# Kernel optimization log

Measured on AMD Instinct MI355X. Metric: run time of the kernel, lower is better.

Reference implementation:

```python
import jax, jax.numpy as jnp
import numpy as np

B, N_OBS = 4096, 64
H = 256
SCALE = 0.05  # keep activations stable through SQUARE/MUL layers


def setup_inputs() -> dict:
    key = jax.random.key(0)
    ks = jax.random.split(key, 16)
    rn = lambda k, shp, s=SCALE: s * jax.random.normal(k, shp, dtype=jnp.float32)
    return {
        "x": jax.random.normal(ks[0], (B, N_OBS), dtype=jnp.float32),
        "xdot": jax.random.normal(ks[1], (B, N_OBS), dtype=jnp.float32),
        "w1": rn(ks[2], (H, N_OBS)), "b1": rn(ks[3], (H,)),
        "w2a": rn(ks[4], (H, H)), "b2a": rn(ks[5], (H,)),
        "w2b": rn(ks[6], (H, H)), "b2b": rn(ks[7], (H,)),
        "w3a": rn(ks[8], (H, H)), "b3a": rn(ks[9], (H,)),
        "w3s": rn(ks[10], (H, N_OBS)), "b3s": rn(ks[11], (H,)),
        "wout": rn(ks[12], (1, H)),
        "scalar": jax.random.normal(ks[13], (1,), dtype=jnp.float32),
    }


def reference(x, xdot, w1, b1, w2a, b2a, w2b, b2b, w3a, b3a, w3s, b3s, wout, scalar):
    # mul path: empty mul_activation -> yy = x*0 + scalar  (shape [B, n_obs])
    yy = x * 0 + scalar

    # Layer 1: SQUARE. Initial jac is identity, so
    # matmul(2*diag(z), W1) @ I == 2*z[:,:,None] * W1
    z = x @ w1.T + b1                      # [B, H]
    y = z * z
    jac = (2.0 * z)[:, :, None] * w1[None]  # [B, H, N_OBS]

    # Layer 2: MUL. diag(z1)@W2b + diag(z2)@W2a == z1[:,:,None]*w2b + z2[:,:,None]*w2a
    z1 = y @ w2a.T + b2a
    z2 = y @ w2b.T + b2b
    y = z1 * z2
    grad = z1[:, :, None] * w2b[None] + z2[:, :, None] * w2a[None]  # [B, H, H]
    jac = jnp.einsum('boh,bhi->boi', grad, jac)                      # [B, H, N_OBS]

    # Layer 3: SKIP. jac = diag(z1)@W3s + (diag(z2)@W3a)@jac
    z1 = y @ w3a.T + b3a
    z2 = x @ w3s.T + b3s
    y = z1 * z2
    jac = z1[:, :, None] * w3s[None] + z2[:, :, None] * jnp.einsum('oh,bhi->boi', w3a, jac)

    numerical_b = y @ wout.T                                # [B, 1]
    jac = jnp.einsum('oh,bhi->boi', wout, jac)              # [B, 1, N_OBS]
    numerical_bdot = jnp.sum(jac[:, 0, :] * xdot, axis=1)   # [B]
    return (numerical_b, numerical_bdot, y, yy)
```

## Files before the change

kernel.cpp:

```cpp
#include <hip/hip_runtime.h>

typedef unsigned short ushort_t;
typedef unsigned int uint_t;
typedef __bf16 bf16x8 __attribute__((ext_vector_type(8)));
typedef float f32x4 __attribute__((ext_vector_type(4)));

#define H 256
#define RPB 16
#define NBLK 256

#define NB_OFF 0
#define BDOT_OFF 4096
#define Y_OFF 8192
#define YY_OFF (8192 + 4096 * 256)

__device__ __forceinline__ ushort_t f2bf(float x) {
    union { float f; uint_t u; } c; c.f = x;
    uint_t r = (c.u + 0x7FFFu + ((c.u >> 16) & 1u)) >> 16;
    return (ushort_t)r;
}
__device__ __forceinline__ float bf2f(ushort_t v) {
    union { uint_t u; float f; } c; c.u = ((uint_t)v) << 16;
    return c.f;
}

#define O_W1b  0
#define O_W1T  16384
#define O_W2ab 32768
#define O_W2bb 98304
#define O_W3ab 163840
#define O_W2aT 229376
#define O_W2bT 294912
#define O_W3aT 360448
#define O_W3sb 425984
#define O_W3sT 442368

__global__ __launch_bounds__(256) void prep_weights(
    const float* __restrict__ w1, const float* __restrict__ w2a,
    const float* __restrict__ w2b, const float* __restrict__ w3a,
    const float* __restrict__ w3s, const float* __restrict__ wout,
    ushort_t* __restrict__ ws) {
    __shared__ float tile[32][65];
    int b = blockIdx.x;
    const float* src; int Oo, Ot, C, t; bool scl;
    if (b < 32)       { src = w2a; Oo = O_W2ab; Ot = O_W2aT; C = 256; t = b;       scl = false; }
    else if (b < 64)  { src = w2b; Oo = O_W2bb; Ot = O_W2bT; C = 256; t = b - 32;  scl = false; }
    else if (b < 96)  { src = w3a; Oo = O_W3ab; Ot = O_W3aT; C = 256; t = b - 64;  scl = true;  }
    else if (b < 104) { src = w1;  Oo = O_W1b;  Ot = O_W1T;  C = 64;  t = b - 96;  scl = false; }
    else              { src = w3s; Oo = O_W3sb; Ot = O_W3sT; C = 64;  t = b - 104; scl = true;  }
    int tr, tc;
    if (C == 256) { tr = t >> 2; tc = t & 3; } else { tr = t; tc = 0; }
    int r0 = tr * 32, c0 = tc * 64;
    const int tid = threadIdx.x;

    union pack8 { ushort_t u[8]; uint4 q; };
    {
        int r = tid >> 3, c8 = (tid & 7) << 3;
        const float* s = src + (r0 + r) * C + c0 + c8;
        pack8 p;
#pragma unroll
        for (int j = 0; j < 8; j++) { float v = s[j]; tile[r][c8 + j] = v; p.u[j] = f2bf(v); }
        *(uint4*)(ws + Oo + (r0 + r) * C + c0 + c8) = p.q;
    }
    __syncthreads();
    {
        int cc = tid >> 2, r8 = (tid & 3) << 3;
        pack8 p;
#pragma unroll
        for (int j = 0; j < 8; j++) {
            float v = tile[r8 + j][cc];
            if (scl) v *= wout[r0 + r8 + j];
            p.u[j] = f2bf(v);
        }
        *(uint4*)(ws + Ot + (c0 + cc) * 256 + r0 + r8) = p.q;
    }
}

#define U_BA   0
#define U_BB   16384
#define U_Z    32768
#define U_Y    36864
#define U_Z12  40960
#define U_Z22  45056
#define U_Z13  49152
#define U_Z23  53248
#define U_U    57344
#define U_XD   61440
#define U_NB   63488
#define SMEM_USHORTS 63520
#define SMEM_BYTES (SMEM_USHORTS * 2)

__device__ __forceinline__ void gload16(const ushort_t* g, ushort_t* l) {
    __builtin_amdgcn_global_load_lds(
        (const __attribute__((address_space(1))) void*)g,
        (__attribute__((address_space(3))) void*)l, 16, 0, 0);
}

__device__ __forceinline__ int posw(int r, int c) { return r * H + (c ^ ((r & 7) << 3)); }

template <bool SUM>
__device__ __forceinline__ void staged_dual(
    const ushort_t* __restrict__ g0, const ushort_t* __restrict__ g1,
    const ushort_t* sA0, const ushort_t* sA1,
    ushort_t* sB0, ushort_t* sB1,
    int wid, int lane, f32x4& acc0, f32x4& acc1) {
    const int nsrc = (wid << 4) + (lane >> 2);
    const int osrc = ((lane & 3) ^ (nsrc & 3)) << 3;
    const ushort_t* s0 = g0 + nsrc * 256 + osrc;
    const ushort_t* s1 = g1 + nsrc * 256 + osrc;
    const int dstb = wid << 9;
    const int row = lane & 15;
    const int nn = (wid << 4) + row;
    const int kq = (lane >> 4) << 3;
    const int boff = nn * 32 + (kq ^ ((nn & 3) << 3));
    const int sw = (row & 7) << 3;
    const ushort_t* a0p = sA0 + row * 256;
    const ushort_t* a1p = sA1 + row * 256;

    asm volatile("s_waitcnt vmcnt(0)" ::: "memory");
    gload16(s0, sB0 + dstb);
    gload16(s1, sB1 + dstb);
    gload16(s0 + 32, sB0 + 8192 + dstb);
    gload16(s1 + 32, sB1 + 8192 + dstb);
#pragma unroll
    for (int c = 0; c < 8; ++c) {
        if (c < 7) asm volatile("s_waitcnt vmcnt(2)" ::: "memory");
        else       asm volatile("s_waitcnt vmcnt(0)" ::: "memory");
        const int cb = (c & 1) << 13;
        bf16x8 a0 = *(const bf16x8*)(a0p + (((c << 5) + kq) ^ sw));
        bf16x8 b0 = *(const bf16x8*)(sB0 + cb + boff);
        bf16x8 a1 = *(const bf16x8*)(a1p + (((c << 5) + kq) ^ sw));
        bf16x8 b1 = *(const bf16x8*)(sB1 + cb + boff);
        if (c < 6) {
            asm volatile("s_waitcnt lgkmcnt(0)" ::: "memory");
            gload16(s0 + (c + 2) * 32, sB0 + cb + dstb);
            gload16(s1 + (c + 2) * 32, sB1 + cb + dstb);
        }
        acc0 = __builtin_amdgcn_mfma_f32_16x16x32_bf16(a0, b0, acc0, 0, 0, 0);
        if (SUM)
            acc0 = __builtin_amdgcn_mfma_f32_16x16x32_bf16(a1, b1, acc0, 0, 0, 0);
        else
            acc1 = __builtin_amdgcn_mfma_f32_16x16x32_bf16(a1, b1, acc1, 0, 0, 0);
    }
}

template <int NF, int STRA, int STRB>
__device__ __forceinline__ void gemm_one(const ushort_t* sA, const ushort_t* __restrict__ B0,
                                         int lane, int k0, f32x4& acc0) {
    const int row = lane & 15;
    const int kq = (lane >> 4) << 3;
    const int sw = (row & 7) << 3;
    bf16x8 b0[NF], a[NF];
    const ushort_t* bp0 = B0 + row * STRB + k0 + kq;
    const ushort_t* ap = sA + row * STRA;
#pragma unroll
    for (int i = 0; i < NF; i++) b0[i] = *(const bf16x8*)(bp0 + i * 32);
#pragma unroll
    for (int i = 0; i < NF; i++) a[i] = *(const bf16x8*)(ap + ((k0 + i * 32 + kq) ^ sw));
    __builtin_amdgcn_sched_barrier(0);
#pragma unroll
    for (int i = 0; i < NF; i++)
        acc0 = __builtin_amdgcn_mfma_f32_16x16x32_bf16(a[i], b0[i], acc0, 0, 0, 0);
}

__global__ __launch_bounds__(1024) void net_main(
    const float* __restrict__ x, const float* __restrict__ xd,
    const float* __restrict__ b1, const float* __restrict__ b2a,
    const float* __restrict__ b2b, const float* __restrict__ b3a,
    const float* __restrict__ b3s, const float* __restrict__ wout,
    const float* __restrict__ scalar, const ushort_t* __restrict__ ws,
    float* __restrict__ out) {
    extern __shared__ __align__(16) ushort_t smem[];
    ushort_t* sBA = smem + U_BA;
    ushort_t* sBB = smem + U_BB;
    ushort_t* sZ  = smem + U_Z;
    ushort_t* sY  = smem + U_Y;
    ushort_t* sZ12 = smem + U_Z12;
    ushort_t* sZ22 = smem + U_Z22;
    ushort_t* sZ13 = smem + U_Z13;
    ushort_t* sZ23 = smem + U_Z23;
    ushort_t* sU  = smem + U_U;
    float* sXd = (float*)(smem + U_XD);
    float* sNB = (float*)(smem + U_NB);

    const int tid = threadIdx.x;
    const int wid = tid >> 6;
    const int lane = tid & 63;
    const int row16 = lane & 15;
    const int rq = lane >> 4;
    const int R0 = blockIdx.x * RPB;
    const int n0 = wid * 16;
    const int row = lane & 15;
    const int kq = (lane >> 4) << 3;
    const int sw = (row & 7) << 3;

    {
        const ushort_t* w1p = ws + O_W1b + (n0 + row) * 64 + kq;
        const ushort_t* w3p = ws + O_W3sb + (n0 + row) * 64 + kq;
        bf16x8 pb0 = *(const bf16x8*)(w1p);
        bf16x8 pb1 = *(const bf16x8*)(w1p + 32);
        bf16x8 pb2 = *(const bf16x8*)(w3p);
        bf16x8 pb3 = *(const bf16x8*)(w3p + 32);
        const float* xg = x + (R0 + row) * 64;
        float4 x0 = *(const float4*)(xg + kq);
        float4 x1 = *(const float4*)(xg + kq + 4);
        float4 x2 = *(const float4*)(xg + 32 + kq);
        float4 x3 = *(const float4*)(xg + 32 + kq + 4);
        float sc = scalar[0];
        {
            int r = tid >> 6, c = tid & 63;
            sXd[tid] = xd[(R0 + r) * 64 + c];
            out[YY_OFF + (R0 + r) * 64 + c] = sc;
            if (tid < RPB) sNB[tid] = 0.f;
        }
        union { ushort_t u[8]; bf16x8 v; } A0, A1;
#pragma unroll
        for (int j = 0; j < 4; j++) {
            A0.u[j]     = f2bf(((const float*)&x0)[j]);
            A0.u[4 + j] = f2bf(((const float*)&x1)[j]);
            A1.u[j]     = f2bf(((const float*)&x2)[j]);
            A1.u[4 + j] = f2bf(((const float*)&x3)[j]);
        }
        f32x4 z = {0.f,0.f,0.f,0.f}, q = {0.f,0.f,0.f,0.f};
        z = __builtin_amdgcn_mfma_f32_16x16x32_bf16(A0.v, pb0, z, 0, 0, 0);
        z = __builtin_amdgcn_mfma_f32_16x16x32_bf16(A1.v, pb1, z, 0, 0, 0);
        q = __builtin_amdgcn_mfma_f32_16x16x32_bf16(A0.v, pb2, q, 0, 0, 0);
        q = __builtin_amdgcn_mfma_f32_16x16x32_bf16(A1.v, pb3, q, 0, 0, 0);
        int c = n0 + row16;
        float bz = b1[c], bs = b3s[c];
#pragma unroll
        for (int i = 0; i < 4; i++) {
            int r = rq * 4 + i;
            int p = posw(r, c);
            float za = z[i] + bz;
            sZ[p] = f2bf(za);
            sY[p] = f2bf(za * za);
            sZ23[p] = f2bf(q[i] + bs);
        }
    }
    __syncthreads();

    {
        f32x4 aA = {0.f,0.f,0.f,0.f}, aB = {0.f,0.f,0.f,0.f};
        staged_dual<false>(ws + O_W2ab, ws + O_W2bb, sY, sY, sBA, sBB, wid, lane, aA, aB);
        int c = n0 + row16;
        float ba = b2a[c], bb = b2b[c];
#pragma unroll
        for (int i = 0; i < 4; i++) {
            int r = rq * 4 + i;
            int p = posw(r, c);
            float z12 = aA[i] + ba, z22 = aB[i] + bb;
            sZ12[p] = f2bf(z12);
            sZ22[p] = f2bf(z22);
            sU[p] = f2bf(z12 * z22);
        }
    }
    __syncthreads();

    {
        f32x4 zz = {0.f,0.f,0.f,0.f}, tt = {0.f,0.f,0.f,0.f};
        staged_dual<false>(ws + O_W3ab, ws + O_W3aT, sU, sZ23, sBA, sBB, wid, lane, zz, tt);
        int c = n0 + row16;
        float ba = b3a[c], wo = wout[c];
#pragma unroll
        for (int i = 0; i < 4; i++) {
            int r = rq * 4 + i;
            int p = posw(r, c);
            float z13 = zz[i] + ba;
            float z23 = bf2f(sZ23[p]);
            float y3 = z13 * z23;
            out[Y_OFF + (R0 + r) * H + c] = y3;
            sZ13[p] = f2bf(z13);
            float t = tt[i];
            sZ12[p] = f2bf(t * bf2f(sZ12[p]));
            sZ22[p] = f2bf(t * bf2f(sZ22[p]));
            float v = wo * y3;
            v += __shfl_xor(v, 1);
            v += __shfl_xor(v, 2);
            v += __shfl_xor(v, 4);
            v += __shfl_xor(v, 8);
            if (row16 == 0) atomicAdd(&sNB[r], v);
        }
    }
    __syncthreads();

    {
        f32x4 pp = {0.f,0.f,0.f,0.f}, dummy = {0.f,0.f,0.f,0.f};
        staged_dual<true>(ws + O_W2bT, ws + O_W2aT, sZ12, sZ22, sBA, sBB, wid, lane, pp, dummy);
        int c = n0 + row16;
#pragma unroll
        for (int i = 0; i < 4; i++) {
            int r = rq * 4 + i;
            int p = posw(r, c);
            sZ[p] = f2bf(2.f * pp[i] * bf2f(sZ[p]));
        }
    }
    __syncthreads();

    {
        int mat = wid >> 3, kh = (wid >> 2) & 1, nt = wid & 3;
        const ushort_t* A = mat ? sZ : sZ13;
        const ushort_t* B = ws + (mat ? O_W1T : O_W3sT) + nt * 16 * H;
        f32x4 acc = {0.f,0.f,0.f,0.f};
        gemm_one<4, H, H>(A, B, lane, kh * 128, acc);
        float* dst = mat ? ((float*)sU + kh * 1024) : ((float*)sY + kh * 1024);
        int c = nt * 16 + row16;
#pragma unroll
        for (int i = 0; i < 4; i++) dst[(rq * 4 + i) * 64 + c] = acc[i];
    }
    __syncthreads();

    {
        float* F0 = (float*)sY;
        float* F1 = F0 + 1024;
        float* F2 = (float*)sU;
        float* F3 = F2 + 1024;
        int r = tid >> 6, j = tid & 63;
        int e = r * 64 + j;
        float s = (F0[e] + F1[e] + F2[e] + F3[e]) * sXd[e];
        s += __shfl_xor(s, 1);
        s += __shfl_xor(s, 2);
        s += __shfl_xor(s, 4);
        s += __shfl_xor(s, 8);
        s += __shfl_xor(s, 16);
        s += __shfl_xor(s, 32);
        if (j == 0) out[BDOT_OFF + R0 + r] = s;
        if (tid < RPB) out[NB_OFF + R0 + tid] = sNB[tid];
    }
}

extern "C" void kernel_launch(void* const* d_in, const int* in_sizes, int n_in,
                              void* d_out, int out_size, void* d_ws, size_t ws_size,
                              hipStream_t stream) {
    (void)in_sizes; (void)n_in; (void)out_size; (void)ws_size;
    const float* x = (const float*)d_in[0];
    const float* xd = (const float*)d_in[1];
    const float* w1 = (const float*)d_in[2];
    const float* b1 = (const float*)d_in[3];
    const float* w2a = (const float*)d_in[4];
    const float* b2a = (const float*)d_in[5];
    const float* w2b = (const float*)d_in[6];
    const float* b2b = (const float*)d_in[7];
    const float* w3a = (const float*)d_in[8];
    const float* b3a = (const float*)d_in[9];
    const float* w3s = (const float*)d_in[10];
    const float* b3s = (const float*)d_in[11];
    const float* wout = (const float*)d_in[12];
    const float* scalar = (const float*)d_in[13];
    ushort_t* ws = (ushort_t*)d_ws;
    float* out = (float*)d_out;

    static bool attr_set = false;
    if (!attr_set) {
        hipFuncSetAttribute((const void*)net_main,
                            hipFuncAttributeMaxDynamicSharedMemorySize, SMEM_BYTES);
        attr_set = true;
    }

    prep_weights<<<112, 256, 0, stream>>>(w1, w2a, w2b, w3a, w3s, wout, ws);
    net_main<<<NBLK, 1024, SMEM_BYTES, stream>>>(x, xd, b1, b2a, b2b, b3a, b3s, wout, scalar, ws, out);
}
```

Baseline: 30.51 us.

## Replace per-phase double-buffered weight staging with cross-phase per-wave LDS ring

Swaps the per-phase double-buffered shared staging of weight tiles for a per-wave five-slot LDS ring that keeps four 16-byte async global-to-LDS loads in flight. The ring runs continuously across the three GEMM phases, so the next phase's weights are prefetched while the current phase computes. The first weight loads are issued before layer 1, and the y3 global store is deferred to the end of the kernel. __syncthreads is replaced by a lighter lgkmcnt wait plus a raw s_barrier. The goal is to hide global-load latency and phase-start stalls, at the cost of more LDS use and fragile hand-managed vmcnt accounting.

Result: slower. 31.21 us (+2.3%).

```diff
diff --git a/kernel.cpp b/kernel.cpp
--- a/kernel.cpp
+++ b/kernel.cpp
@@ -76,18 +76,18 @@
     }
 }
 
-#define U_BA   0
-#define U_BB   16384
-#define U_Z    32768
-#define U_Y    36864
-#define U_Z12  40960
-#define U_Z22  45056
-#define U_Z13  49152
-#define U_Z23  53248
-#define U_U    57344
-#define U_XD   61440
-#define U_NB   63488
-#define SMEM_USHORTS 63520
+#define RS 5
+#define RA 4
+#define U_RING 0
+#define U_Z    40960
+#define U_Y    45056
+#define U_Z12  49152
+#define U_Z22  53248
+#define U_Z23  57344
+#define U_U    61440
+#define U_XD   65536
+#define U_NB   69632
+#define SMEM_USHORTS 69664
 #define SMEM_BYTES (SMEM_USHORTS * 2)
 
 __device__ __forceinline__ void gload16(const ushort_t* g, ushort_t* l) {
@@ -96,51 +96,59 @@
         (__attribute__((address_space(3))) void*)l, 16, 0, 0);
 }
 
+template <int N> __device__ __forceinline__ void vwait() {
+    if constexpr (N == 3) asm volatile("s_waitcnt vmcnt(3)" ::: "memory");
+    else if constexpr (N == 2) asm volatile("s_waitcnt vmcnt(2)" ::: "memory");
+    else if constexpr (N == 1) asm volatile("s_waitcnt vmcnt(1)" ::: "memory");
+    else asm volatile("s_waitcnt vmcnt(0)" ::: "memory");
+}
+
+#define PHASE_BARRIER() do { \
+    asm volatile("s_waitcnt lgkmcnt(0)" ::: "memory"); \
+    __builtin_amdgcn_sched_barrier(0); \
+    __builtin_amdgcn_s_barrier(); \
+    __builtin_amdgcn_sched_barrier(0); \
+} while (0)
+
 __device__ __forceinline__ int posw(int r, int c) { return r * H + (c ^ ((r & 7) << 3)); }
 
-template <bool SUM>
-__device__ __forceinline__ void staged_dual(
-    const ushort_t* __restrict__ g0, const ushort_t* __restrict__ g1,
-    const ushort_t* sA0, const ushort_t* sA1,
-    ushort_t* sB0, ushort_t* sB1,
-    int wid, int lane, f32x4& acc0, f32x4& acc1) {
-    const int nsrc = (wid << 4) + (lane >> 2);
-    const int osrc = ((lane & 3) ^ (nsrc & 3)) << 3;
-    const ushort_t* s0 = g0 + nsrc * 256 + osrc;
-    const ushort_t* s1 = g1 + nsrc * 256 + osrc;
-    const int dstb = wid << 9;
-    const int row = lane & 15;
-    const int nn = (wid << 4) + row;
-    const int kq = (lane >> 4) << 3;
-    const int boff = nn * 32 + (kq ^ ((nn & 3) << 3));
-    const int sw = (row & 7) << 3;
-    const ushort_t* a0p = sA0 + row * 256;
-    const ushort_t* a1p = sA1 + row * 256;
-
-    asm volatile("s_waitcnt vmcnt(0)" ::: "memory");
-    gload16(s0, sB0 + dstb);
-    gload16(s1, sB1 + dstb);
-    gload16(s0 + 32, sB0 + 8192 + dstb);
-    gload16(s1 + 32, sB1 + 8192 + dstb);
-#pragma unroll
-    for (int c = 0; c < 8; ++c) {
-        if (c < 7) asm volatile("s_waitcnt vmcnt(2)" ::: "memory");
-        else       asm volatile("s_waitcnt vmcnt(0)" ::: "memory");
-        const int cb = (c & 1) << 13;
-        bf16x8 a0 = *(const bf16x8*)(a0p + (((c << 5) + kq) ^ sw));
-        bf16x8 b0 = *(const bf16x8*)(sB0 + cb + boff);
-        bf16x8 a1 = *(const bf16x8*)(a1p + (((c << 5) + kq) ^ sw));
-        bf16x8 b1 = *(const bf16x8*)(sB1 + cb + boff);
-        if (c < 6) {
-            asm volatile("s_waitcnt lgkmcnt(0)" ::: "memory");
-            gload16(s0 + (c + 2) * 32, sB0 + cb + dstb);
-            gload16(s1 + (c + 2) * 32, sB1 + cb + dstb);
-        }
-        acc0 = __builtin_amdgcn_mfma_f32_16x16x32_bf16(a0, b0, acc0, 0, 0, 0);
+template <int P, bool SUM>
+__device__ __forceinline__ void ring_phase(
+    const ushort_t* __restrict__ gm0, const ushort_t* __restrict__ gm1,
+    const ushort_t* __restrict__ gn0, const ushort_t* __restrict__ gn1,
+    const ushort_t* aP0, const ushort_t* aP1,
+    ushort_t* rw, int srcoff, int boff, int kq, int sw,
+    f32x4& acc0, f32x4& acc1) {
+#pragma unroll
+    for (int k = 0; k < 16; ++k) {
+        const int u = P * 16 + k;
+        if (P == 2) {
+            if (k < 13) vwait<3>();
+            else if (k == 13) vwait<2>();
+            else if (k == 14) vwait<1>();
+            else vwait<0>();
+        } else {
+            vwait<3>();
+        }
+        __builtin_amdgcn_sched_barrier(0);
+        bf16x8 b = *(const bf16x8*)(rw + (u % RS) * 512 + boff);
+        const ushort_t* ap = (k & 1) ? aP1 : aP0;
+        bf16x8 a = *(const bf16x8*)(ap + ((((k >> 1) << 5) + kq) ^ sw));
+        if (u + RA < 48) {
+            asm volatile("s_waitcnt lgkmcnt(2)" ::: "memory");
+            __builtin_amdgcn_sched_barrier(0);
+            const int k4 = k + RA;
+            const ushort_t* g = (k4 < 16) ? ((k4 & 1) ? gm1 : gm0)
+                                          : ((k4 & 1) ? gn1 : gn0);
+            const int cc = (k4 & 15) >> 1;
+            gload16(g + srcoff + (cc << 5), rw + ((u + RA) % RS) * 512);
+        }
         if (SUM)
-            acc0 = __builtin_amdgcn_mfma_f32_16x16x32_bf16(a1, b1, acc0, 0, 0, 0);
+            acc0 = __builtin_amdgcn_mfma_f32_16x16x32_bf16(a, b, acc0, 0, 0, 0);
+        else if ((k & 1) == 0)
+            acc0 = __builtin_amdgcn_mfma_f32_16x16x32_bf16(a, b, acc0, 0, 0, 0);
         else
-            acc1 = __builtin_amdgcn_mfma_f32_16x16x32_bf16(a1, b1, acc1, 0, 0, 0);
+            acc1 = __builtin_amdgcn_mfma_f32_16x16x32_bf16(a, b, acc1, 0, 0, 0);
     }
 }
 
@@ -171,15 +179,12 @@
     const float* __restrict__ scalar, const ushort_t* __restrict__ ws,
     float* __restrict__ out) {
     extern __shared__ __align__(16) ushort_t smem[];
-    ushort_t* sBA = smem + U_BA;
-    ushort_t* sBB = smem + U_BB;
-    ushort_t* sZ  = smem + U_Z;
-    ushort_t* sY  = smem + U_Y;
+    ushort_t* sZ   = smem + U_Z;
+    ushort_t* sY   = smem + U_Y;
     ushort_t* sZ12 = smem + U_Z12;
     ushort_t* sZ22 = smem + U_Z22;
-    ushort_t* sZ13 = smem + U_Z13;
     ushort_t* sZ23 = smem + U_Z23;
-    ushort_t* sU  = smem + U_U;
+    ushort_t* sU   = smem + U_U;
     float* sXd = (float*)(smem + U_XD);
     float* sNB = (float*)(smem + U_NB);
 
@@ -190,29 +195,44 @@
     const int rq = lane >> 4;
     const int R0 = blockIdx.x * RPB;
     const int n0 = wid * 16;
-    const int row = lane & 15;
-    const int kq = (lane >> 4) << 3;
-    const int sw = (row & 7) << 3;
-
-    {
-        const ushort_t* w1p = ws + O_W1b + (n0 + row) * 64 + kq;
-        const ushort_t* w3p = ws + O_W3sb + (n0 + row) * 64 + kq;
+    const int kq = rq << 3;
+    const int sw = (row16 & 7) << 3;
+
+    ushort_t* rw = smem + U_RING + wid * (RS * 512);
+    const int srcoff = ((wid << 4) + (lane >> 2)) * 256 + (lane & 3) * 8;
+    const int boff = row16 * 32 + rq * 8;
+
+    const ushort_t* gW2ab = ws + O_W2ab;
+    const ushort_t* gW2bb = ws + O_W2bb;
+    const ushort_t* gW3ab = ws + O_W3ab;
+    const ushort_t* gW3aT = ws + O_W3aT;
+    const ushort_t* gW2bT = ws + O_W2bT;
+    const ushort_t* gW2aT = ws + O_W2aT;
+
+    f32x4 y3keep;
+    {
+        const ushort_t* w1p = ws + O_W1b + (n0 + row16) * 64 + kq;
+        const ushort_t* w3p = ws + O_W3sb + (n0 + row16) * 64 + kq;
         bf16x8 pb0 = *(const bf16x8*)(w1p);
         bf16x8 pb1 = *(const bf16x8*)(w1p + 32);
         bf16x8 pb2 = *(const bf16x8*)(w3p);
         bf16x8 pb3 = *(const bf16x8*)(w3p + 32);
-        const float* xg = x + (R0 + row) * 64;
+        const float* xg = x + (R0 + row16) * 64;
         float4 x0 = *(const float4*)(xg + kq);
         float4 x1 = *(const float4*)(xg + kq + 4);
         float4 x2 = *(const float4*)(xg + 32 + kq);
         float4 x3 = *(const float4*)(xg + 32 + kq + 4);
+        int xr = tid >> 6, xc = tid & 63;
+        float xdv = xd[(R0 + xr) * 64 + xc];
         float sc = scalar[0];
-        {
-            int r = tid >> 6, c = tid & 63;
-            sXd[tid] = xd[(R0 + r) * 64 + c];
-            out[YY_OFF + (R0 + r) * 64 + c] = sc;
-            if (tid < RPB) sNB[tid] = 0.f;
-        }
+        gload16(gW2ab + srcoff, rw);
+        gload16(gW2bb + srcoff, rw + 512);
+        gload16(gW2ab + srcoff + 32, rw + 1024);
+        gload16(gW2bb + srcoff + 32, rw + 1536);
+        __builtin_amdgcn_sched_barrier(0);
+        out[YY_OFF + (R0 + xr) * 64 + xc] = sc;
+        sXd[tid] = xdv;
+        if (tid < RPB) sNB[tid] = 0.f;
         union { ushort_t u[8]; bf16x8 v; } A0, A1;
 #pragma unroll
         for (int j = 0; j < 4; j++) {
@@ -238,11 +258,16 @@
             sZ23[p] = f2bf(q[i] + bs);
         }
     }
-    __syncthreads();
+    PHASE_BARRIER();
+
+    const ushort_t* aRow = (const ushort_t*)0;
+    (void)aRow;
+    const int arow = row16 * H;
 
     {
         f32x4 aA = {0.f,0.f,0.f,0.f}, aB = {0.f,0.f,0.f,0.f};
-        staged_dual<false>(ws + O_W2ab, ws + O_W2bb, sY, sY, sBA, sBB, wid, lane, aA, aB);
+        ring_phase<0, false>(gW2ab, gW2bb, gW3ab, gW3aT, sY + arow, sY + arow,
+                             rw, srcoff, boff, kq, sw, aA, aB);
         int c = n0 + row16;
         float ba = b2a[c], bb = b2b[c];
 #pragma unroll
@@ -255,11 +280,12 @@
             sU[p] = f2bf(z12 * z22);
         }
     }
-    __syncthreads();
+    PHASE_BARRIER();
 
     {
         f32x4 zz = {0.f,0.f,0.f,0.f}, tt = {0.f,0.f,0.f,0.f};
-        staged_dual<false>(ws + O_W3ab, ws + O_W3aT, sU, sZ23, sBA, sBB, wid, lane, zz, tt);
+        ring_phase<1, false>(gW3ab, gW3aT, gW2bT, gW2aT, sU + arow, sZ23 + arow,
+                             rw, srcoff, boff, kq, sw, zz, tt);
         int c = n0 + row16;
         float ba = b3a[c], wo = wout[c];
 #pragma unroll
@@ -269,8 +295,8 @@
             float z13 = zz[i] + ba;
             float z23 = bf2f(sZ23[p]);
             float y3 = z13 * z23;
-            out[Y_OFF + (R0 + r) * H + c] = y3;
-            sZ13[p] = f2bf(z13);
+            y3keep[i] = y3;
+            sY[p] = f2bf(z13);
             float t = tt[i];
             sZ12[p] = f2bf(t * bf2f(sZ12[p]));
             sZ22[p] = f2bf(t * bf2f(sZ22[p]));
@@ -282,11 +308,12 @@
             if (row16 == 0) atomicAdd(&sNB[r], v);
         }
     }
-    __syncthreads();
+    PHASE_BARRIER();
 
     {
         f32x4 pp = {0.f,0.f,0.f,0.f}, dummy = {0.f,0.f,0.f,0.f};
-        staged_dual<true>(ws + O_W2bT, ws + O_W2aT, sZ12, sZ22, sBA, sBB, wid, lane, pp, dummy);
+        ring_phase<2, true>(gW2bT, gW2aT, gW2bT, gW2aT, sZ12 + arow, sZ22 + arow,
+                            rw, srcoff, boff, kq, sw, pp, dummy);
         int c = n0 + row16;
 #pragma unroll
         for (int i = 0; i < 4; i++) {
@@ -295,23 +322,29 @@
             sZ[p] = f2bf(2.f * pp[i] * bf2f(sZ[p]));
         }
     }
-    __syncthreads();
-
-    {
+    PHASE_BARRIER();
+
+    {
+        int c = n0 + row16;
+#pragma unroll
+        for (int i = 0; i < 4; i++)
+            out[Y_OFF + (R0 + rq * 4 + i) * H + c] = y3keep[i];
         int mat = wid >> 3, kh = (wid >> 2) & 1, nt = wid & 3;
-        const ushort_t* A = mat ? sZ : sZ13;
+        const ushort_t* A = mat ? sZ : sY;
         const ushort_t* B = ws + (mat ? O_W1T : O_W3sT) + nt * 16 * H;
         f32x4 acc = {0.f,0.f,0.f,0.f};
         gemm_one<4, H, H>(A, B, lane, kh * 128, acc);
-        float* dst = mat ? ((float*)sU + kh * 1024) : ((float*)sY + kh * 1024);
-        int c = nt * 16 + row16;
-#pragma unroll
-        for (int i = 0; i < 4; i++) dst[(rq * 4 + i) * 64 + c] = acc[i];
-    }
-    __syncthreads();
-
-    {
-        float* F0 = (float*)sY;
+        float* F01 = (float*)sZ23;
+        float* F23 = (float*)sU;
+        float* dst = mat ? (F23 + kh * 1024) : (F01 + kh * 1024);
+        int cc = nt * 16 + row16;
+#pragma unroll
+        for (int i = 0; i < 4; i++) dst[(rq * 4 + i) * 64 + cc] = acc[i];
+    }
+    PHASE_BARRIER();
+
+    {
+        float* F0 = (float*)sZ23;
         float* F1 = F0 + 1024;
         float* F2 = (float*)sU;
         float* F3 = F2 + 1024;
```
